# Kernel tuning notes

Hardware: AMD Instinct MI355X
Metric: run time of the kernel (lower is better)

## Reference

```python
import jax, jax.numpy as jnp
import numpy as np

NUM_HEADS = 8
NEG_SLOPE = 0.2


def setup_inputs() -> dict:
    key = jax.random.key(0)
    k1, k2, k3, k4 = jax.random.split(key, 4)
    B, N, D_IN, D_K, D_V = 4, 4096, 256, 256, 256
    x = jax.random.normal(k1, (B, N, D_IN), dtype=jnp.float32)
    Wq = jax.random.normal(k2, (D_IN, D_K), dtype=jnp.float32) * (1.0 / np.sqrt(D_IN))
    Wk = jax.random.normal(k3, (D_IN, D_K), dtype=jnp.float32) * (1.0 / np.sqrt(D_IN))
    Wv = jax.random.normal(k4, (D_IN, D_V), dtype=jnp.float32) * (1.0 / np.sqrt(D_IN))
    return {"x": x, "Wq": Wq, "Wk": Wk, "Wv": Wv}


def reference(x, Wq, Wk, Wv):
    B, N, _ = x.shape
    nh = NUM_HEADS
    dim_k = Wq.shape[1]
    dim_v = Wv.shape[1]
    dk, dv = dim_k // nh, dim_v // nh
    nor_fact = 1.0 / np.sqrt(dk)
    # project and split heads: [B, H, N, dk]
    q = (x @ Wq).reshape(B, N, nh, dk).transpose(0, 2, 1, 3)
    k = (x @ Wk).reshape(B, N, nh, dk).transpose(0, 2, 1, 3)
    v = (x @ Wv).reshape(B, N, nh, dv).transpose(0, 2, 1, 3)
    # all-pairs scores, scaled then LeakyReLU (no softmax)
    dist = jnp.einsum('bhnd,bhmd->bhnm', q, k) * nor_fact
    dist = jnp.where(dist >= 0, dist, NEG_SLOPE * dist)
    att = jnp.einsum('bhnm,bhmd->bhnd', dist, v)
    return att.transpose(0, 2, 1, 3).reshape(B, N, dim_v)
```

## Files before the change

### kernel.cpp

```cpp
#include <hip/hip_runtime.h>

typedef __attribute__((ext_vector_type(8))) short short8;
typedef __attribute__((ext_vector_type(4))) float f32x4;
typedef __attribute__((ext_vector_type(2))) unsigned int u32x2;
typedef __attribute__((ext_vector_type(4))) unsigned int u32x4;

#define MFMA16x32(A, B, C) \
  __builtin_amdgcn_mfma_f32_16x16x32_bf16((A), (B), (C), 0, 0, 0)

__device__ __forceinline__ void async_cp16(const unsigned short* g, void* l) {
  __builtin_amdgcn_global_load_lds(
      (const __attribute__((address_space(1))) unsigned int*)g,
      (__attribute__((address_space(3))) unsigned int*)l, 16, 0, 0);
}

__device__ __forceinline__ unsigned int fbits(float f) {
  return __builtin_bit_cast(unsigned int, f);
}
__device__ __forceinline__ unsigned int pack_bf16(float a, float b) {
  return __builtin_amdgcn_perm(fbits(b), fbits(a), 0x07060302u);
}
__device__ __forceinline__ unsigned short bf16_rne(float f) {
  unsigned int u = fbits(f);
  return (unsigned short)((u + 0x8000u) >> 16);
}
__device__ __forceinline__ unsigned int relu_pk_bf16(unsigned int x) {
  unsigned int r;
  asm("v_pk_max_i16 %0, %1, 0" : "=v"(r) : "v"(x));
  return r;
}

__global__ __launch_bounds__(256) void prep_kernel(
    const float* __restrict__ x, unsigned short* __restrict__ xb,
    const float* __restrict__ Wq, const float* __restrict__ Wk,
    const float* __restrict__ Wv, unsigned short* __restrict__ WT) {
  __shared__ float tile[32][33];
  if (blockIdx.x < 4096) {
    const size_t i = ((size_t)blockIdx.x * 256 + threadIdx.x) * 4;
    const float4 f = *(const float4*)(x + i);
    u32x2 u = {(unsigned int)bf16_rne(f.x) | ((unsigned int)bf16_rne(f.y) << 16),
               (unsigned int)bf16_rne(f.z) | ((unsigned int)bf16_rne(f.w) << 16)};
    *(u32x2*)(xb + i) = u;
    return;
  }
  const int bid = blockIdx.x - 4096;
  const int g = bid / 64, rem = bid % 64;
  const int k0 = (rem >> 3) * 32, n0 = (rem & 7) * 32;
  const float* W = (g == 0) ? Wq : (g == 1) ? Wk : Wv;
  const int t = threadIdx.x;
  {
    const int kr = t >> 3, nc = (t & 7) * 4;
    const float4 f = *(const float4*)(W + (size_t)(k0 + kr) * 256 + n0 + nc);
    tile[kr][nc + 0] = f.x; tile[kr][nc + 1] = f.y;
    tile[kr][nc + 2] = f.z; tile[kr][nc + 3] = f.w;
  }
  __syncthreads();
  {
    const int nr = t >> 3, kc = (t & 7) * 4;
    unsigned int u0 = (unsigned int)bf16_rne(tile[kc + 0][nr]) |
                      ((unsigned int)bf16_rne(tile[kc + 1][nr]) << 16);
    unsigned int u1 = (unsigned int)bf16_rne(tile[kc + 2][nr]) |
                      ((unsigned int)bf16_rne(tile[kc + 3][nr]) << 16);
    u32x2 u = {u0, u1};
    *(u32x2*)(WT + (size_t)g * 65536 + (size_t)(n0 + nr) * 256 + k0 + kc) = u;
  }
}

__global__ __launch_bounds__(256, 2) void proj_kernel(
    const unsigned short* __restrict__ xb, const unsigned short* __restrict__ WT,
    unsigned short* __restrict__ QH, unsigned short* __restrict__ KH,
    unsigned short* __restrict__ VT) {
  __shared__ __align__(16) char smem[65536];
  const int tid = threadIdx.x;
  const int w = tid >> 6, lane = tid & 63, l15 = lane & 15, quad = lane >> 4;
  const int bid = blockIdx.x;
  const int mtile = bid / 6, nt = bid % 6;
  const int g = nt >> 1, n0 = (nt & 1) * 128;
  const int m0 = mtile * 128;

  const int srow = lane >> 3, useg = lane & 7;
  const int swz = (useg ^ srow) * 8;
  const unsigned short* aS = xb + (size_t)(m0 + w * 32 + srow) * 256 + swz;
  const unsigned short* bS =
      WT + (size_t)g * 65536 + (size_t)(n0 + w * 32 + srow) * 256 + swz;

#pragma unroll
  for (int j = 0; j < 4; j++) {
    async_cp16(aS + j * 2048, smem + w * 4096 + j * 1024);
    async_cp16(bS + j * 2048, smem + 16384 + w * 4096 + j * 1024);
  }
  __syncthreads();

  const f32x4 zero = {0.f, 0.f, 0.f, 0.f};
  f32x4 acc[2][8];
#pragma unroll
  for (int s = 0; s < 2; s++)
#pragma unroll
    for (int c = 0; c < 8; c++) acc[s][c] = zero;

  const int sw = l15 & 7;
  for (int t = 0; t < 4; t++) {
    const int nb = t & 1;
    const int kn = ((t + 1) & 3) * 64;
#pragma unroll
    for (int j = 0; j < 4; j++) {
      async_cp16(aS + kn + j * 2048,
                 smem + (nb ^ 1) * 32768 + w * 4096 + j * 1024);
      async_cp16(bS + kn + j * 2048,
                 smem + (nb ^ 1) * 32768 + 16384 + w * 4096 + j * 1024);
    }
    const char* Ab = smem + nb * 32768;
    const char* Bb = Ab + 16384;
#pragma unroll
    for (int ks = 0; ks < 2; ks++) {
      const int seg = ((ks * 4 + quad) ^ sw) * 16;
      short8 af[2], bf[8];
#pragma unroll
      for (int s = 0; s < 2; s++)
        af[s] = *(const short8*)(Ab + (w * 32 + s * 16 + l15) * 128 + seg);
#pragma unroll
      for (int c = 0; c < 8; c++)
        bf[c] = *(const short8*)(Bb + (c * 16 + l15) * 128 + seg);
      if (g < 2) {
#pragma unroll
        for (int s = 0; s < 2; s++)
#pragma unroll
          for (int c = 0; c < 8; c++)
            acc[s][c] = MFMA16x32(bf[c], af[s], acc[s][c]);
      } else {
#pragma unroll
        for (int s = 0; s < 2; s++)
#pragma unroll
          for (int c = 0; c < 8; c++)
            acc[s][c] = MFMA16x32(af[s], bf[c], acc[s][c]);
      }
    }
    __syncthreads();
  }

  if (g < 2) {
    unsigned short* O = g ? KH : QH;
    const float sc = g ? 1.0f : 0.17677669529663688f;
#pragma unroll
    for (int s = 0; s < 2; s++)
#pragma unroll
      for (int c = 0; c < 8; c++) {
        const int row = m0 + w * 32 + s * 16 + l15;
        const int col = n0 + c * 16 + quad * 4;
        const int bb = row >> 12, nn = row & 4095;
        const int hh = col >> 5, dl = col & 31;
        u32x2 pk = {pack_bf16(acc[s][c][0] * sc, acc[s][c][1] * sc),
                    pack_bf16(acc[s][c][2] * sc, acc[s][c][3] * sc)};
        *(u32x2*)(O + ((size_t)(bb * 8 + hh) * 4096 + nn) * 32 + dl) = pk;
      }
  } else {
#pragma unroll
    for (int s = 0; s < 2; s++)
#pragma unroll
      for (int c = 0; c < 8; c++) {
        const int col = n0 + c * 16 + l15;
        const int hh = col >> 5, dl = col & 31;
        const int row = m0 + w * 32 + s * 16 + quad * 4;
        const int bb = row >> 12;
        const int nn = (row & 4064) | (quad << 3) | ((s & 1) << 2);
        u32x2 pk = {pack_bf16(acc[s][c][0], acc[s][c][1]),
                    pack_bf16(acc[s][c][2], acc[s][c][3])};
        *(u32x2*)(VT + (size_t)((bb * 8 + hh) * 32 + dl) * 4096 + nn) = pk;
      }
  }
}

__global__ __launch_bounds__(512, 4) void attn_kernel(
    const unsigned short* __restrict__ QH, const unsigned short* __restrict__ KH,
    const unsigned short* __restrict__ VT, float* __restrict__ out) {
  __shared__ __align__(16) char smem[32768];
  const int tid = threadIdx.x;
  const int w = tid >> 6, lane = tid & 63, l15 = lane & 15, quad = lane >> 4;
  const int bid = blockIdx.x;
  const int bh = bid & 31, qh = bid >> 5;
  const int b = bh >> 3, h = bh & 7;
  const int qbase = qh * 256 + w * 32;

  const unsigned short* Qp =
      QH + ((size_t)bh * 4096 + qbase + l15) * 32 + quad * 8;
  short8 qf[2];
#pragma unroll
  for (int s = 0; s < 2; s++) qf[s] = *(const short8*)(Qp + (size_t)s * 512);

  const f32x4 zero = {0.f, 0.f, 0.f, 0.f};

  float* Mred = (float*)smem;
  {
    f32x4 mm[2][2];
#pragma unroll
    for (int dt = 0; dt < 2; dt++)
#pragma unroll
      for (int it = 0; it < 2; it++) mm[dt][it] = zero;
    const unsigned short* Vg = VT + ((size_t)bh * 32 + l15) * 4096 + quad * 8;
    const unsigned short* Kg = KH + ((size_t)bh * 4096) * 32 + l15;
    for (int g = 0; g < 16; g++) {
      const int kb = w * 512 + g * 32;
      short8 va[2];
#pragma unroll
      for (int dt = 0; dt < 2; dt++)
        va[dt] = *(const short8*)(Vg + (size_t)dt * 16 * 4096 + kb);
      short8 kv[2];
#pragma unroll
      for (int it = 0; it < 2; it++) {
        unsigned short t[8];
#pragma unroll
        for (int j = 0; j < 8; j++)
          t[j] = Kg[(size_t)(kb + (j >> 2) * 16 + quad * 4 + (j & 3)) * 32 +
                    it * 16];
        kv[it] = *(const short8*)t;
      }
#pragma unroll
      for (int dt = 0; dt < 2; dt++)
#pragma unroll
        for (int it = 0; it < 2; it++)
          mm[dt][it] = MFMA16x32(va[dt], kv[it], mm[dt][it]);
    }
#pragma unroll
    for (int dt = 0; dt < 2; dt++)
#pragma unroll
      for (int it = 0; it < 2; it++)
#pragma unroll
        for (int r = 0; r < 4; r++)
          Mred[w * 1024 + (dt * 16 + quad * 4 + r) * 32 + it * 16 + l15] =
              mm[dt][it][r];
  }
  __syncthreads();
  short8 ma[2];
  {
#pragma unroll
    for (int dt = 0; dt < 2; dt++) {
      f32x4 sa = zero, sb = zero;
#pragma unroll
      for (int ww = 0; ww < 8; ww++) {
        const float* p = Mred + ww * 1024 + (dt * 16 + l15) * 32 + quad * 8;
        sa += *(const f32x4*)p;
        sb += *(const f32x4*)(p + 4);
      }
      u32x4 mw = {pack_bf16(sa[0], sa[1]), pack_bf16(sa[2], sa[3]),
                  pack_bf16(sb[0], sb[1]), pack_bf16(sb[2], sb[3])};
      ma[dt] = __builtin_bit_cast(short8, mw);
    }
  }
  __syncthreads();

  const bool isK = (w < 4);
  const unsigned short* src0;
  int kstr, wbOff;
  if (isK) {
    const int key = w * 16 + (lane >> 2);
    const int gseg = (lane & 3) ^ ((lane >> 3) & 3);
    src0 = KH + ((size_t)bh * 4096 + key) * 32 + gseg * 8;
    kstr = 32;
    wbOff = w * 1024;
  } else {
    const int r = (w - 4) * 8 + (lane >> 3), useg = lane & 7;
    src0 = VT + ((size_t)bh * 32 + r) * 4096 + ((useg ^ (r & 7)) * 8);
    kstr = 1;
    wbOff = 4096 + (w - 4) * 1024;
  }

  async_cp16(src0, smem + wbOff);
  __syncthreads();

  f32x4 acc[2][2];
#pragma unroll
  for (int s = 0; s < 2; s++) {
    acc[s][0] = zero;
    acc[s][1] = zero;
  }

  const int rs = l15 & 7;
  const int kseg = (quad ^ ((l15 >> 1) & 3)) * 16;
  for (int i = 0; i < 64; i++) {
    const int nb = i & 1;
    const int kn = ((i + 1) & 63) * 64;
    async_cp16(src0 + (size_t)kn * kstr, smem + (nb ^ 1) * 8192 + wbOff);

    const char* Kb = smem + nb * 8192;
    const char* Vb = Kb + 4096;
    short8 kf[4];
#pragma unroll
    for (int c = 0; c < 4; c++)
      kf[c] = *(const short8*)(Kb + (c * 16 + l15) * 64 + kseg);
    short8 vf[2][2];
#pragma unroll
    for (int dt = 0; dt < 2; dt++) {
      const char* Vr = Vb + (dt * 16 + l15) * 128;
#pragma unroll
      for (int u = 0; u < 2; u++)
        vf[dt][u] = *(const short8*)(Vr + (((4 * u + quad) ^ rs) * 16));
    }

#pragma unroll
    for (int s = 0; s < 2; s++) {
      unsigned int pp[4][2];
#pragma unroll
      for (int c = 0; c < 4; c++) {
        f32x4 st = MFMA16x32(kf[c], qf[s], zero);
        pp[c][0] = relu_pk_bf16(pack_bf16(st[0], st[1]));
        pp[c][1] = relu_pk_bf16(pack_bf16(st[2], st[3]));
      }
#pragma unroll
      for (int u = 0; u < 2; u++) {
        u32x4 bw = {pp[2 * u][0], pp[2 * u][1],
                    pp[2 * u + 1][0], pp[2 * u + 1][1]};
        short8 pb = __builtin_bit_cast(short8, bw);
#pragma unroll
        for (int dt = 0; dt < 2; dt++)
          acc[s][dt] = MFMA16x32(vf[dt][u], pb, acc[s][dt]);
      }
    }
    __syncthreads();
  }

#pragma unroll
  for (int s = 0; s < 2; s++)
#pragma unroll
    for (int dt = 0; dt < 2; dt++) {
      f32x4 corr = MFMA16x32(ma[dt], qf[s], zero);
      f32x4 o = acc[s][dt] * 0.8f + corr * 0.2f;
      *(f32x4*)(out + ((size_t)b * 4096 + qbase + s * 16 + l15) * 256 + h * 32 +
                dt * 16 + quad * 4) = o;
    }
}

extern "C" void kernel_launch(void* const* d_in, const int* in_sizes, int n_in,
                              void* d_out, int out_size, void* d_ws,
                              size_t ws_size, hipStream_t stream) {
  const float* x = (const float*)d_in[0];
  const float* Wq = (const float*)d_in[1];
  const float* Wk = (const float*)d_in[2];
  const float* Wv = (const float*)d_in[3];
  float* out = (float*)d_out;

  unsigned short* ws = (unsigned short*)d_ws;
  unsigned short* QHb = ws;
  unsigned short* KHb = ws + 4194304;
  unsigned short* VTb = ws + 2 * 4194304;
  unsigned short* xbb = ws + 3 * 4194304;
  unsigned short* WTb = ws + 4 * 4194304;

  prep_kernel<<<4288, 256, 0, stream>>>(x, xbb, Wq, Wk, Wv, WTb);
  proj_kernel<<<768, 256, 0, stream>>>(xbb, WTb, QHb, KHb, VTb);
  attn_kernel<<<512, 512, 0, stream>>>(QHb, KHb, VTb, out);
}
```

Baseline: 180.6 us.

## Precompute per-head V^T K matrix in separate kernel instead of per block

Moves the per-(batch,head) reduction of V^T·K over all keys out of the attention kernel into a dedicated kernel that runs once per head and writes a bf16 matrix to workspace. Attention blocks then load this precomputed matrix instead of each recomputing it, removing 16x redundant work and halving their LDS use. The trade-off is an extra launch and a small 32-block kernel with low GPU occupancy on the critical path.

After: 155.2 us. 1.16x faster.

```diff
diff --git a/kernel.cpp b/kernel.cpp
--- a/kernel.cpp
+++ b/kernel.cpp
@@ -170,10 +170,75 @@
   }
 }
 
+__global__ __launch_bounds__(512) void mkv_kernel(
+    const unsigned short* __restrict__ KH, const unsigned short* __restrict__ VT,
+    unsigned short* __restrict__ MW) {
+  __shared__ __align__(16) float Mred[8][32][32];
+  const int tid = threadIdx.x;
+  const int w = tid >> 6, lane = tid & 63, l15 = lane & 15, quad = lane >> 4;
+  const int bh = blockIdx.x;
+
+  const f32x4 zero = {0.f, 0.f, 0.f, 0.f};
+  f32x4 mm[2][2];
+#pragma unroll
+  for (int dt = 0; dt < 2; dt++)
+#pragma unroll
+    for (int it = 0; it < 2; it++) mm[dt][it] = zero;
+
+  const unsigned short* Vg = VT + ((size_t)bh * 32 + l15) * 4096 + quad * 8;
+  const unsigned short* Kg = KH + (size_t)bh * 4096 * 32;
+
+  for (int g = 0; g < 16; g++) {
+    const int kb = w * 512 + g * 32;
+    short8 va[2];
+#pragma unroll
+    for (int dt = 0; dt < 2; dt++)
+      va[dt] = *(const short8*)(Vg + (size_t)dt * 16 * 4096 + kb);
+    short8 kv0, kv1;
+#pragma unroll
+    for (int j = 0; j < 8; j++) {
+      const int key = kb + ((j >> 2) << 4) + quad * 4 + (j & 3);
+      const size_t base = (size_t)key * 32 + l15;
+      kv0[j] = (short)Kg[base];
+      kv1[j] = (short)Kg[base + 16];
+    }
+#pragma unroll
+    for (int dt = 0; dt < 2; dt++) {
+      mm[dt][0] = MFMA16x32(va[dt], kv0, mm[dt][0]);
+      mm[dt][1] = MFMA16x32(va[dt], kv1, mm[dt][1]);
+    }
+  }
+#pragma unroll
+  for (int dt = 0; dt < 2; dt++)
+#pragma unroll
+    for (int it = 0; it < 2; it++)
+#pragma unroll
+      for (int r = 0; r < 4; r++)
+        Mred[w][dt * 16 + quad * 4 + r][it * 16 + l15] = mm[dt][it][r];
+  __syncthreads();
+
+  if (w == 0) {
+#pragma unroll
+    for (int dt = 0; dt < 2; dt++) {
+      f32x4 sa = zero, sb = zero;
+#pragma unroll
+      for (int ww = 0; ww < 8; ww++) {
+        const float* p = &Mred[ww][dt * 16 + l15][quad * 8];
+        sa += *(const f32x4*)p;
+        sb += *(const f32x4*)(p + 4);
+      }
+      u32x4 mw = {pack_bf16(sa[0], sa[1]), pack_bf16(sa[2], sa[3]),
+                  pack_bf16(sb[0], sb[1]), pack_bf16(sb[2], sb[3])};
+      *(u32x4*)(MW + (size_t)bh * 1024 + dt * 512 + lane * 8) = mw;
+    }
+  }
+}
+
 __global__ __launch_bounds__(512, 4) void attn_kernel(
     const unsigned short* __restrict__ QH, const unsigned short* __restrict__ KH,
-    const unsigned short* __restrict__ VT, float* __restrict__ out) {
-  __shared__ __align__(16) char smem[32768];
+    const unsigned short* __restrict__ VT, const unsigned short* __restrict__ MW,
+    float* __restrict__ out) {
+  __shared__ __align__(16) char smem[16384];
   const int tid = threadIdx.x;
   const int w = tid >> 6, lane = tid & 63, l15 = lane & 15, quad = lane >> 4;
   const int bid = blockIdx.x;
@@ -187,66 +252,10 @@
 #pragma unroll
   for (int s = 0; s < 2; s++) qf[s] = *(const short8*)(Qp + (size_t)s * 512);
 
-  const f32x4 zero = {0.f, 0.f, 0.f, 0.f};
-
-  float* Mred = (float*)smem;
-  {
-    f32x4 mm[2][2];
-#pragma unroll
-    for (int dt = 0; dt < 2; dt++)
-#pragma unroll
-      for (int it = 0; it < 2; it++) mm[dt][it] = zero;
-    const unsigned short* Vg = VT + ((size_t)bh * 32 + l15) * 4096 + quad * 8;
-    const unsigned short* Kg = KH + ((size_t)bh * 4096) * 32 + l15;
-    for (int g = 0; g < 16; g++) {
-      const int kb = w * 512 + g * 32;
-      short8 va[2];
-#pragma unroll
-      for (int dt = 0; dt < 2; dt++)
-        va[dt] = *(const short8*)(Vg + (size_t)dt * 16 * 4096 + kb);
-      short8 kv[2];
-#pragma unroll
-      for (int it = 0; it < 2; it++) {
-        unsigned short t[8];
-#pragma unroll
-        for (int j = 0; j < 8; j++)
-          t[j] = Kg[(size_t)(kb + (j >> 2) * 16 + quad * 4 + (j & 3)) * 32 +
-                    it * 16];
-        kv[it] = *(const short8*)t;
-      }
-#pragma unroll
-      for (int dt = 0; dt < 2; dt++)
-#pragma unroll
-        for (int it = 0; it < 2; it++)
-          mm[dt][it] = MFMA16x32(va[dt], kv[it], mm[dt][it]);
-    }
-#pragma unroll
-    for (int dt = 0; dt < 2; dt++)
-#pragma unroll
-      for (int it = 0; it < 2; it++)
-#pragma unroll
-        for (int r = 0; r < 4; r++)
-          Mred[w * 1024 + (dt * 16 + quad * 4 + r) * 32 + it * 16 + l15] =
-              mm[dt][it][r];
-  }
-  __syncthreads();
   short8 ma[2];
-  {
-#pragma unroll
-    for (int dt = 0; dt < 2; dt++) {
-      f32x4 sa = zero, sb = zero;
-#pragma unroll
-      for (int ww = 0; ww < 8; ww++) {
-        const float* p = Mred + ww * 1024 + (dt * 16 + l15) * 32 + quad * 8;
-        sa += *(const f32x4*)p;
-        sb += *(const f32x4*)(p + 4);
-      }
-      u32x4 mw = {pack_bf16(sa[0], sa[1]), pack_bf16(sa[2], sa[3]),
-                  pack_bf16(sb[0], sb[1]), pack_bf16(sb[2], sb[3])};
-      ma[dt] = __builtin_bit_cast(short8, mw);
-    }
-  }
-  __syncthreads();
+#pragma unroll
+  for (int dt = 0; dt < 2; dt++)
+    ma[dt] = *(const short8*)(MW + (size_t)bh * 1024 + dt * 512 + lane * 8);
 
   const bool isK = (w < 4);
   const unsigned short* src0;
@@ -267,6 +276,7 @@
   async_cp16(src0, smem + wbOff);
   __syncthreads();
 
+  const f32x4 zero = {0.f, 0.f, 0.f, 0.f};
   f32x4 acc[2][2];
 #pragma unroll
   for (int s = 0; s < 2; s++) {
@@ -344,8 +354,10 @@
   unsigned short* VTb = ws + 2 * 4194304;
   unsigned short* xbb = ws + 3 * 4194304;
   unsigned short* WTb = ws + 4 * 4194304;
+  unsigned short* MWb = WTb + 196608;
 
   prep_kernel<<<4288, 256, 0, stream>>>(x, xbb, Wq, Wk, Wv, WTb);
   proj_kernel<<<768, 256, 0, stream>>>(xbb, WTb, QHb, KHb, VTb);
-  attn_kernel<<<512, 512, 0, stream>>>(QHb, KHb, VTb, out);
-}
+  mkv_kernel<<<32, 512, 0, stream>>>(KHb, VTb, MWb);
+  attn_kernel<<<512, 512, 0, stream>>>(QHb, KHb, VTb, MWb, out);
+}
```
